# Optimization experiments

Measured on AMD Instinct MI355X. Metric: run time of the kernel, lower is better.

## Reference

```python
import jax, jax.numpy as jnp
import numpy as np

IN_DIMS = 1024
K = 8


def setup_inputs() -> dict:
    key = jax.random.key(0)
    ks = jax.random.split(key, 7)
    s = 1.0 / np.sqrt(IN_DIMS)
    x = jax.random.normal(ks[0], (8, 2048, IN_DIMS), dtype=jnp.float32)
    Wq = jax.random.uniform(ks[1], (IN_DIMS, K), jnp.float32, -s, s)
    bq = jax.random.uniform(ks[2], (K,), jnp.float32, -s, s)
    Wk = jax.random.uniform(ks[3], (IN_DIMS, K), jnp.float32, -s, s)
    bk = jax.random.uniform(ks[4], (K,), jnp.float32, -s, s)
    Wv = jax.random.uniform(ks[5], (IN_DIMS, IN_DIMS), jnp.float32, -s, s)
    bv = jax.random.uniform(ks[6], (IN_DIMS,), jnp.float32, -s, s)
    return {"x": x, "Wq": Wq, "bq": bq, "Wk": Wk, "bk": bk, "Wv": Wv, "bv": bv}


def reference(x, Wq, bq, Wk, bk, Wv, bv):
    # x: [B,S,D]; rank-k projections
    q = jnp.einsum('bsd,dk->bsk', x, Wq) + bq        # [B,S,k]
    k = jnp.einsum('bsd,dk->bsk', x, Wk) + bk        # [B,S,k]
    energy = jnp.einsum('bik,bjk->bij', q, k)        # [B,S,S] (unscaled)
    attention = jax.nn.softmax(energy, axis=-1)
    value = jnp.einsum('bsd,de->bse', x, Wv) + bv    # [B,S,D]
    out = jnp.einsum('bij,bjd->bid', attention, value)
    return (out, attention)
```

## Files before the change

### kernel.cpp

```cpp
#include <hip/hip_runtime.h>


typedef __attribute__((ext_vector_type(8))) __bf16 bf16x8;
typedef __attribute__((ext_vector_type(4))) __bf16 bf16x4;
typedef __attribute__((ext_vector_type(4))) float  f32x4;
typedef unsigned int u32;

#define GLB_CAST(p) ((const __attribute__((address_space(1))) u32*)(p))
#define LDS_CAST(p) ((__attribute__((address_space(3))) u32*)(p))

#define S_BARRIER() { __builtin_amdgcn_s_barrier(); __builtin_amdgcn_sched_barrier(0); }
#define LGKM0()     { asm volatile("s_waitcnt lgkmcnt(0)" ::: "memory"); __builtin_amdgcn_sched_barrier(0); }
#define VMCNT8()    { asm volatile("s_waitcnt vmcnt(8)" ::: "memory"); __builtin_amdgcn_sched_barrier(0); }
#define VMCNT0()    { asm volatile("s_waitcnt vmcnt(0)" ::: "memory"); __builtin_amdgcn_sched_barrier(0); }

static constexpr int    Bn   = 8;
static constexpr int    S    = 2048;
static constexpr int    Dd   = 1024;
static constexpr int    Mtot = Bn * S;
static constexpr size_t OUT0 = (size_t)Bn * S * Dd;

static constexpr size_t OFF_XBF  = 0;
static constexpr size_t OFF_WVT  = OFF_XBF + (size_t)Mtot * Dd * 2;
static constexpr size_t OFF_WQKT = OFF_WVT + (size_t)Dd * Dd * 2;
static constexpr size_t OFF_Q    = OFF_WQKT + (size_t)16 * Dd * 2;
static constexpr size_t OFF_K    = OFF_Q   + (size_t)Mtot * 8 * 4;
static constexpr size_t OFF_VT   = OFF_K   + (size_t)Mtot * 8 * 4;
static constexpr size_t OFF_ATTB = OFF_VT  + (size_t)Bn * Dd * S * 2;
static constexpr size_t WS_NEED  = OFF_ATTB + (size_t)Bn * S * S * 2;

__global__ __launch_bounds__(256) void prep_kernel(
    const float* __restrict__ x, const float* __restrict__ Wq,
    const float* __restrict__ Wk, const float* __restrict__ Wv,
    __bf16* __restrict__ xbf, __bf16* __restrict__ wvt, __bf16* __restrict__ wqkT)
{
    __shared__ float lt[64][65];
    int bid = blockIdx.x, t = threadIdx.x;
    if (bid < 4096) {
        #pragma unroll
        for (int i = 0; i < 4; ++i) {
            size_t idx4 = (size_t)i * 1048576 + (size_t)bid * 256 + t;
            f32x4 v = ((const f32x4*)x)[idx4];
            bf16x4 o;
            #pragma unroll
            for (int c = 0; c < 4; ++c) o[c] = (__bf16)v[c];
            ((bf16x4*)xbf)[idx4] = o;
        }
    } else if (bid < 4352) {
        int tile = bid - 4096;
        int tr = tile >> 4, tc = tile & 15;
        int r0 = t >> 6, c = t & 63;
        #pragma unroll
        for (int i = 0; i < 16; ++i) {
            int row = i * 4 + r0;
            lt[row][c] = Wv[(size_t)(tr * 64 + row) * 1024 + tc * 64 + c];
        }
        __syncthreads();
        #pragma unroll
        for (int i = 0; i < 16; ++i) {
            int er = i * 4 + r0;
            wvt[(size_t)(tc * 64 + er) * 1024 + tr * 64 + c] = (__bf16)lt[c][er];
        }
    } else {
        int lb = bid - 4352;
        #pragma unroll
        for (int i = 0; i < 4; ++i) {
            int idx = (lb * 4 + i) * 256 + t;
            int n = idx >> 10, d = idx & 1023;
            float v = (n < 8) ? Wq[d * 8 + n] : Wk[d * 8 + (n & 7)];
            wqkT[n * 1024 + d] = (__bf16)v;
        }
    }
}

__global__ __launch_bounds__(256) void qk_proj_kernel(
    const __bf16* __restrict__ xbf, const __bf16* __restrict__ wqkT,
    const float* __restrict__ bq, const float* __restrict__ bk,
    float* __restrict__ qb, float* __restrict__ kb)
{
    int t = threadIdx.x, l = t & 63, w = t >> 6;
    int mbase = (blockIdx.x * 4 + w) * 16;
    f32x4 acc = {0.f, 0.f, 0.f, 0.f};
    const __bf16* ar = xbf + (size_t)(mbase + (l & 15)) * 1024 + ((l >> 4) << 3);
    const __bf16* br = wqkT + (size_t)(l & 15) * 1024 + ((l >> 4) << 3);
    #pragma unroll 8
    for (int kk = 0; kk < 1024; kk += 32) {
        bf16x8 a = *(const bf16x8*)(ar + kk);
        bf16x8 b = *(const bf16x8*)(br + kk);
        acc = __builtin_amdgcn_mfma_f32_16x16x32_bf16(a, b, acc, 0, 0, 0);
    }
    int n = l & 15;
    float bias = (n < 8) ? bq[n] : bk[n & 7];
    #pragma unroll
    for (int r = 0; r < 4; ++r) {
        int m = mbase + ((l >> 4) << 2) + r;
        float v = acc[r] + bias;
        if (n < 8) qb[m * 8 + n] = v;
        else       kb[m * 8 + (n & 7)] = v;
    }
}

__global__ __launch_bounds__(256) void fused_gs_kernel(
    const __bf16* __restrict__ xbf, const __bf16* __restrict__ wvt,
    const float* __restrict__ bv,
    const float* __restrict__ qb, const float* __restrict__ kb,
    __bf16* __restrict__ vtOut, float* __restrict__ attnF,
    __bf16* __restrict__ attnB)
{
    __shared__ __align__(1024) char smem[32768];
    __shared__ float redm[4], reds[4];
    int bid = blockIdx.x, t = threadIdx.x;
    int seg = bid >> 8;
    int gid = -1, sid = -1;
    if (seg == 0) gid = bid;
    else if (seg == 1) sid = bid - 256;
    else if (seg == 2) gid = bid - 256;
    else if (seg == 3) sid = bid - 512;
    else gid = bid - 512;

    if (sid < 0) {
        int g = ((gid & 7) << 7) | (gid >> 3);
        int mblk = g >> 3, nblk = g & 7;
        int l = t & 63, wid = t >> 6;
        int wmr = wid >> 1, wnc = wid & 1;
        int lr = l & 15, lk = l >> 4;

        int srow = t >> 3;
        int ssl  = (t & 7) ^ (srow & 7);
        const __bf16* gA = xbf + (size_t)(mblk * 128 + srow) * 1024 + ssl * 8;
        const __bf16* gB = wvt + (size_t)(nblk * 128 + srow) * 1024 + ssl * 8;

        int s0 = (lk ^ (lr & 7)) << 3;
        int s1 = ((lk ^ 4) ^ (lr & 7)) << 3;
        int offA0 = (wmr * 64 + lr) * 64 + s0;
        int offA1 = (wmr * 64 + lr) * 64 + s1;
        int offB0 = (wnc * 64 + lr) * 64 + s0;
        int offB1 = (wnc * 64 + lr) * 64 + s1;

        f32x4 acc[4][4] = {};

        for (int tt = 0; tt < 16; ++tt) {
            int kk = tt * 64;
            #pragma unroll
            for (int c = 0; c < 4; ++c) {
                __builtin_amdgcn_global_load_lds(
                    GLB_CAST(gA + (size_t)c * 32 * 1024 + kk),
                    LDS_CAST(smem + c * 4096 + wid * 1024), 16, 0, 0);
                __builtin_amdgcn_global_load_lds(
                    GLB_CAST(gB + (size_t)c * 32 * 1024 + kk),
                    LDS_CAST(smem + 16384 + c * 4096 + wid * 1024), 16, 0, 0);
            }
            __syncthreads();
            const __bf16* As = (const __bf16*)smem;
            const __bf16* Bs = (const __bf16*)(smem + 16384);
            bf16x8 af[4], bfr[4];
            #pragma unroll
            for (int i = 0; i < 4; ++i) af[i]  = *(const bf16x8*)(As + offA0 + i * 1024);
            #pragma unroll
            for (int j = 0; j < 4; ++j) bfr[j] = *(const bf16x8*)(Bs + offB0 + j * 1024);
            #pragma unroll
            for (int i = 0; i < 4; ++i)
                #pragma unroll
                for (int j = 0; j < 4; ++j)
                    acc[i][j] = __builtin_amdgcn_mfma_f32_16x16x32_bf16(af[i], bfr[j], acc[i][j], 0, 0, 0);
            #pragma unroll
            for (int i = 0; i < 4; ++i) af[i]  = *(const bf16x8*)(As + offA1 + i * 1024);
            #pragma unroll
            for (int j = 0; j < 4; ++j) bfr[j] = *(const bf16x8*)(Bs + offB1 + j * 1024);
            #pragma unroll
            for (int i = 0; i < 4; ++i)
                #pragma unroll
                for (int j = 0; j < 4; ++j)
                    acc[i][j] = __builtin_amdgcn_mfma_f32_16x16x32_bf16(af[i], bfr[j], acc[i][j], 0, 0, 0);
            __syncthreads();
        }

        #pragma unroll
        for (int j = 0; j < 4; ++j) {
            int e = (nblk << 7) + wnc * 64 + j * 16 + lr;
            float bias = bv[e];
            #pragma unroll
            for (int i = 0; i < 4; ++i) {
                int m0 = (mblk << 7) + wmr * 64 + i * 16 + (lk << 2);
                int b = m0 >> 11, sA = m0 & 2047;
                bf16x4 o;
                #pragma unroll
                for (int r = 0; r < 4; ++r) o[r] = (__bf16)(acc[i][j][r] + bias);
                *(bf16x4*)&vtOut[(((size_t)(b << 10) + e) << 11) + sA] = o;
            }
        }
    } else {
        int b = sid >> 6, chunk = sid & 63;
        int l = t & 63, w = t >> 6;
        float kr[8][8];
        const float* kbb = kb + ((size_t)b << 14);
        #pragma unroll
        for (int jj = 0; jj < 8; ++jj) {
            f32x4 v0 = *(const f32x4*)(kbb + (size_t)(t * 8 + jj) * 8);
            f32x4 v1 = *(const f32x4*)(kbb + (size_t)(t * 8 + jj) * 8 + 4);
            #pragma unroll
            for (int c = 0; c < 4; ++c) { kr[jj][c] = v0[c]; kr[jj][4 + c] = v1[c]; }
        }
        const float* qrow = qb + ((size_t)b << 14);
        for (int ii = 0; ii < 32; ++ii) {
            int i = (chunk << 5) + ii;
            f32x4 q0 = *(const f32x4*)(qrow + (size_t)i * 8);
            f32x4 q1 = *(const f32x4*)(qrow + (size_t)i * 8 + 4);
            float e[8];
            #pragma unroll
            for (int jj = 0; jj < 8; ++jj) {
                float s = q0[0] * kr[jj][0];
                s = fmaf(q0[1], kr[jj][1], s);
                s = fmaf(q0[2], kr[jj][2], s);
                s = fmaf(q0[3], kr[jj][3], s);
                s = fmaf(q1[0], kr[jj][4], s);
                s = fmaf(q1[1], kr[jj][5], s);
                s = fmaf(q1[2], kr[jj][6], s);
                s = fmaf(q1[3], kr[jj][7], s);
                e[jj] = s;
            }
            float mx = e[0];
            #pragma unroll
            for (int jj = 1; jj < 8; ++jj) mx = fmaxf(mx, e[jj]);
            #pragma unroll
            for (int d = 1; d < 64; d <<= 1) mx = fmaxf(mx, __shfl_xor(mx, d));
            if (l == 0) redm[w] = mx;
            __syncthreads();
            mx = fmaxf(fmaxf(redm[0], redm[1]), fmaxf(redm[2], redm[3]));
            float p[8], sum = 0.f;
            #pragma unroll
            for (int jj = 0; jj < 8; ++jj) { p[jj] = __expf(e[jj] - mx); sum += p[jj]; }
            #pragma unroll
            for (int d = 1; d < 64; d <<= 1) sum += __shfl_xor(sum, d);
            if (l == 0) reds[w] = sum;
            __syncthreads();
            float T = (reds[0] + reds[1]) + (reds[2] + reds[3]);
            float inv = 1.0f / T;
            size_t off = (((size_t)b << 11) + i) * 2048 + (size_t)t * 8;
            f32x4 o0, o1; bf16x8 ob;
            #pragma unroll
            for (int c = 0; c < 4; ++c) {
                o0[c] = p[c] * inv; o1[c] = p[4 + c] * inv;
                ob[c] = (__bf16)o0[c]; ob[4 + c] = (__bf16)o1[c];
            }
            *(f32x4*)(attnF + off) = o0;
            *(f32x4*)(attnF + off + 4) = o1;
            *(bf16x8*)(attnB + off) = ob;
        }
    }
}

__device__ __forceinline__ void g1_stageA(const __bf16* Ab, char* smem,
    int slot, int kk, int c, int rowin, int sl8, int wid)
{
    __builtin_amdgcn_global_load_lds(
        GLB_CAST(Ab + (size_t)(c * 64 + rowin) * 2048 + kk + sl8 * 8),
        LDS_CAST(smem + slot * 65536 + c * 8192 + wid * 1024), 16, 0, 0);
}
__device__ __forceinline__ void g1_stageB(const __bf16* Bb, char* smem,
    int slot, int kk, int c, int rowin, int sl8, int wid)
{
    __builtin_amdgcn_global_load_lds(
        GLB_CAST(Bb + (size_t)(c * 64 + rowin) * 2048 + kk + sl8 * 8),
        LDS_CAST(smem + slot * 65536 + 32768 + c * 8192 + wid * 1024), 16, 0, 0);
}

__global__ __launch_bounds__(512, 2) void gemm1_kernel(
    const __bf16* __restrict__ A, const __bf16* __restrict__ Bt,
    float* __restrict__ outF)
{
    constexpr int NT = 32;
    __shared__ __align__(1024) char smem[131072];

    int bid = blockIdx.x;
    int wg = ((bid & 7) << 5) | (bid >> 3);
    int t = threadIdx.x, l = t & 63;
    int wid = t >> 6;
    int wmr = wid >> 2, wnc = wid & 3;

    int bb = wg >> 5; int r = wg & 31;
    int mblk = r >> 2, nblk = r & 3;
    const __bf16* Ab = A + (size_t)bb * S * S + (size_t)mblk * 256 * 2048;
    const __bf16* Bb = Bt + (size_t)bb * Dd * S + (size_t)nblk * 256 * 2048;

    int rowin = t >> 3;
    int sl8 = (t & 7) ^ (rowin & 7);
    int lr = l & 15, lk = l >> 4;

    f32x4 acc[8][4] = {};

    #pragma unroll
    for (int c = 0; c < 4; ++c) {
        g1_stageA(Ab, smem, 0, 0, c, rowin, sl8, wid);
        g1_stageB(Bb, smem, 0, 0, c, rowin, sl8, wid);
    }
    #pragma unroll
    for (int c = 0; c < 4; ++c) {
        g1_stageA(Ab, smem, 1, 64, c, rowin, sl8, wid);
        g1_stageB(Bb, smem, 1, 64, c, rowin, sl8, wid);
    }
    VMCNT8();
    S_BARRIER();

    for (int tt = 0; tt < NT; ++tt) {
        int s = tt & 1;
        const __bf16* Asl = (const __bf16*)(smem + s * 65536);
        const __bf16* Bsl = (const __bf16*)(smem + s * 65536 + 32768);
        bool pf = (tt + 2 < NT);
        int kk2 = (tt + 2) * 64;

        bf16x8 aLo[2][4], aHi[2][4], bLo[2][2], bHi[2][2];

        #pragma unroll
        for (int ks = 0; ks < 2; ++ks) {
            int sa = ks * 4 + lk;
            #pragma unroll
            for (int i = 0; i < 4; ++i) {
                int ra = wmr * 128 + i * 16 + lr;
                aLo[ks][i] = *(const bf16x8*)&Asl[ra * 64 + ((sa ^ (ra & 7)) << 3)];
            }
            #pragma unroll
            for (int j = 0; j < 2; ++j) {
                int rb = wnc * 64 + j * 16 + lr;
                bLo[ks][j] = *(const bf16x8*)&Bsl[rb * 64 + ((sa ^ (rb & 7)) << 3)];
            }
        }
        S_BARRIER(); LGKM0();
        __builtin_amdgcn_s_setprio(1);
        #pragma unroll
        for (int ks = 0; ks < 2; ++ks)
            #pragma unroll
            for (int i = 0; i < 4; ++i)
                #pragma unroll
                for (int j = 0; j < 2; ++j)
                    acc[i][j] = __builtin_amdgcn_mfma_f32_16x16x32_bf16(aLo[ks][i], bLo[ks][j], acc[i][j], 0, 0, 0);
        __builtin_amdgcn_s_setprio(0);
        S_BARRIER();

        #pragma unroll
        for (int ks = 0; ks < 2; ++ks) {
            int sa = ks * 4 + lk;
            #pragma unroll
            for (int j = 0; j < 2; ++j) {
                int rb = wnc * 64 + (j + 2) * 16 + lr;
                bHi[ks][j] = *(const bf16x8*)&Bsl[rb * 64 + ((sa ^ (rb & 7)) << 3)];
            }
        }
        if (pf) {
            g1_stageA(Ab, smem, s, kk2, 0, rowin, sl8, wid);
            g1_stageA(Ab, smem, s, kk2, 2, rowin, sl8, wid);
        }
        S_BARRIER(); LGKM0();
        __builtin_amdgcn_s_setprio(1);
        #pragma unroll
        for (int ks = 0; ks < 2; ++ks)
            #pragma unroll
            for (int i = 0; i < 4; ++i)
                #pragma unroll
                for (int j = 0; j < 2; ++j)
                    acc[i][2 + j] = __builtin_amdgcn_mfma_f32_16x16x32_bf16(aLo[ks][i], bHi[ks][j], acc[i][2 + j], 0, 0, 0);
        __builtin_amdgcn_s_setprio(0);
        S_BARRIER();

        #pragma unroll
        for (int ks = 0; ks < 2; ++ks) {
            int sa = ks * 4 + lk;
            #pragma unroll
            for (int i = 0; i < 4; ++i) {
                int ra = wmr * 128 + (i + 4) * 16 + lr;
                aHi[ks][i] = *(const bf16x8*)&Asl[ra * 64 + ((sa ^ (ra & 7)) << 3)];
            }
        }
        if (pf) {
            #pragma unroll
            for (int c = 0; c < 4; ++c)
                g1_stageB(Bb, smem, s, kk2, c, rowin, sl8, wid);
        }
        S_BARRIER(); LGKM0();
        __builtin_amdgcn_s_setprio(1);
        #pragma unroll
        for (int ks = 0; ks < 2; ++ks)
            #pragma unroll
            for (int i = 0; i < 4; ++i)
                #pragma unroll
                for (int j = 0; j < 2; ++j)
                    acc[4 + i][2 + j] = __builtin_amdgcn_mfma_f32_16x16x32_bf16(aHi[ks][i], bHi[ks][j], acc[4 + i][2 + j], 0, 0, 0);
        __builtin_amdgcn_s_setprio(0);
        S_BARRIER();

        if (pf) {
            g1_stageA(Ab, smem, s, kk2, 1, rowin, sl8, wid);
            g1_stageA(Ab, smem, s, kk2, 3, rowin, sl8, wid);
        }
        S_BARRIER();
        __builtin_amdgcn_s_setprio(1);
        #pragma unroll
        for (int ks = 0; ks < 2; ++ks)
            #pragma unroll
            for (int i = 0; i < 4; ++i)
                #pragma unroll
                for (int j = 0; j < 2; ++j)
                    acc[4 + i][j] = __builtin_amdgcn_mfma_f32_16x16x32_bf16(aHi[ks][i], bLo[ks][j], acc[4 + i][j], 0, 0, 0);
        __builtin_amdgcn_s_setprio(0);

        if (tt == NT - 1) break;
        S_BARRIER();
        if (pf) { VMCNT8(); } else { VMCNT0(); }
        S_BARRIER();
    }

    float* ob = outF + (size_t)bb * S * Dd;
    #pragma unroll
    for (int i = 0; i < 8; ++i) {
        int m0 = (mblk << 8) + wmr * 128 + i * 16 + (lk << 2);
        #pragma unroll
        for (int j = 0; j < 4; ++j) {
            int e = (nblk << 8) + wnc * 64 + j * 16 + lr;
            #pragma unroll
            for (int r = 0; r < 4; ++r)
                ob[(size_t)(m0 + r) * 1024 + e] = acc[i][j][r];
        }
    }
}

extern "C" void kernel_launch(void* const* d_in, const int* in_sizes, int n_in,
                              void* d_out, int out_size, void* d_ws, size_t ws_size,
                              hipStream_t stream)
{
    const float* x  = (const float*)d_in[0];
    const float* Wq = (const float*)d_in[1];
    const float* bq = (const float*)d_in[2];
    const float* Wk = (const float*)d_in[3];
    const float* bk = (const float*)d_in[4];
    const float* Wv = (const float*)d_in[5];
    const float* bv = (const float*)d_in[6];

    float* outp  = (float*)d_out;
    float* attnF = outp + OUT0;

    if (ws_size < WS_NEED) return;
    char* ws = (char*)d_ws;
    __bf16* xbf   = (__bf16*)(ws + OFF_XBF);
    __bf16* wvt   = (__bf16*)(ws + OFF_WVT);
    __bf16* wqkT  = (__bf16*)(ws + OFF_WQKT);
    float*  qbuf  = (float*)(ws + OFF_Q);
    float*  kbuf  = (float*)(ws + OFF_K);
    __bf16* vt    = (__bf16*)(ws + OFF_VT);
    __bf16* attnB = (__bf16*)(ws + OFF_ATTB);

    prep_kernel<<<4368, 256, 0, stream>>>(x, Wq, Wk, Wv, xbf, wvt, wqkT);
    qk_proj_kernel<<<256, 256, 0, stream>>>(xbf, wqkT, bq, bk, qbuf, kbuf);
    fused_gs_kernel<<<1536, 256, 0, stream>>>(xbf, wvt, bv, qbuf, kbuf, vt, attnF, attnB);
    gemm1_kernel<<<256, 512, 0, stream>>>(attnB, vt, outp);
}
```

Before: 187.1 us.

## Fuse QK projection into prep and overlap fp32 attention writes with gemm

Removes the separate QK projection kernel by computing the rank-16 projection directly from fp32 x inside prep_kernel. The fp32 attention output store is moved out of the softmax kernel into gemm1, which reloads bf16 attention rows and writes them as fp32 while its MFMA loop runs. This aims to hide the large fp32 attention write behind compute and cut a launch, but makes the fp32 attention output carry bf16 rounding and complicates the vmcnt accounting.

```diff
diff --git a/kernel.cpp b/kernel.cpp
--- a/kernel.cpp
+++ b/kernel.cpp
@@ -11,6 +11,7 @@
 
 #define S_BARRIER() { __builtin_amdgcn_s_barrier(); __builtin_amdgcn_sched_barrier(0); }
 #define LGKM0()     { asm volatile("s_waitcnt lgkmcnt(0)" ::: "memory"); __builtin_amdgcn_sched_barrier(0); }
+#define VMCNT9()    { asm volatile("s_waitcnt vmcnt(9)" ::: "memory"); __builtin_amdgcn_sched_barrier(0); }
 #define VMCNT8()    { asm volatile("s_waitcnt vmcnt(8)" ::: "memory"); __builtin_amdgcn_sched_barrier(0); }
 #define VMCNT0()    { asm volatile("s_waitcnt vmcnt(0)" ::: "memory"); __builtin_amdgcn_sched_barrier(0); }
 
@@ -22,8 +23,7 @@
 
 static constexpr size_t OFF_XBF  = 0;
 static constexpr size_t OFF_WVT  = OFF_XBF + (size_t)Mtot * Dd * 2;
-static constexpr size_t OFF_WQKT = OFF_WVT + (size_t)Dd * Dd * 2;
-static constexpr size_t OFF_Q    = OFF_WQKT + (size_t)16 * Dd * 2;
+static constexpr size_t OFF_Q    = OFF_WVT + (size_t)Dd * Dd * 2;
 static constexpr size_t OFF_K    = OFF_Q   + (size_t)Mtot * 8 * 4;
 static constexpr size_t OFF_VT   = OFF_K   + (size_t)Mtot * 8 * 4;
 static constexpr size_t OFF_ATTB = OFF_VT  + (size_t)Bn * Dd * S * 2;
@@ -32,22 +32,41 @@
 __global__ __launch_bounds__(256) void prep_kernel(
     const float* __restrict__ x, const float* __restrict__ Wq,
     const float* __restrict__ Wk, const float* __restrict__ Wv,
-    __bf16* __restrict__ xbf, __bf16* __restrict__ wvt, __bf16* __restrict__ wqkT)
+    const float* __restrict__ bq, const float* __restrict__ bk,
+    __bf16* __restrict__ xbf, __bf16* __restrict__ wvt,
+    float* __restrict__ qb, float* __restrict__ kb)
 {
     __shared__ float lt[64][65];
     int bid = blockIdx.x, t = threadIdx.x;
-    if (bid < 4096) {
-        #pragma unroll
-        for (int i = 0; i < 4; ++i) {
-            size_t idx4 = (size_t)i * 1048576 + (size_t)bid * 256 + t;
-            f32x4 v = ((const f32x4*)x)[idx4];
-            bf16x4 o;
-            #pragma unroll
-            for (int c = 0; c < 4; ++c) o[c] = (__bf16)v[c];
-            ((bf16x4*)xbf)[idx4] = o;
-        }
-    } else if (bid < 4352) {
-        int tile = bid - 4096;
+    if (bid < 256) {
+        int l = t & 63, w = t >> 6;
+        int mbase = (bid * 4 + w) * 16;
+        int n = l & 15;
+        int dbase = (l >> 4) << 3;
+        const float* xr = x + (size_t)(mbase + n) * 1024 + dbase;
+        const float* wcol = (n < 8) ? (Wq + n) : (Wk + (n & 7));
+        f32x4 acc = {0.f, 0.f, 0.f, 0.f};
+        #pragma unroll 4
+        for (int kk = 0; kk < 1024; kk += 32) {
+            f32x4 a0 = *(const f32x4*)(xr + kk);
+            f32x4 a1 = *(const f32x4*)(xr + kk + 4);
+            bf16x8 a, b;
+            #pragma unroll
+            for (int c = 0; c < 4; ++c) { a[c] = (__bf16)a0[c]; a[4 + c] = (__bf16)a1[c]; }
+            #pragma unroll
+            for (int u = 0; u < 8; ++u) b[u] = (__bf16)wcol[(size_t)(dbase + kk + u) * 8];
+            acc = __builtin_amdgcn_mfma_f32_16x16x32_bf16(a, b, acc, 0, 0, 0);
+        }
+        float bias = (n < 8) ? bq[n] : bk[n & 7];
+        #pragma unroll
+        for (int r = 0; r < 4; ++r) {
+            int m = mbase + ((l >> 4) << 2) + r;
+            float v = acc[r] + bias;
+            if (n < 8) qb[m * 8 + n] = v;
+            else       kb[m * 8 + (n & 7)] = v;
+        }
+    } else if (bid < 512) {
+        int tile = bid - 256;
         int tr = tile >> 4, tc = tile & 15;
         int r0 = t >> 6, c = t & 63;
         #pragma unroll
@@ -62,41 +81,16 @@
             wvt[(size_t)(tc * 64 + er) * 1024 + tr * 64 + c] = (__bf16)lt[c][er];
         }
     } else {
-        int lb = bid - 4352;
+        int bid2 = bid - 512;
         #pragma unroll
         for (int i = 0; i < 4; ++i) {
-            int idx = (lb * 4 + i) * 256 + t;
-            int n = idx >> 10, d = idx & 1023;
-            float v = (n < 8) ? Wq[d * 8 + n] : Wk[d * 8 + (n & 7)];
-            wqkT[n * 1024 + d] = (__bf16)v;
-        }
-    }
-}
-
-__global__ __launch_bounds__(256) void qk_proj_kernel(
-    const __bf16* __restrict__ xbf, const __bf16* __restrict__ wqkT,
-    const float* __restrict__ bq, const float* __restrict__ bk,
-    float* __restrict__ qb, float* __restrict__ kb)
-{
-    int t = threadIdx.x, l = t & 63, w = t >> 6;
-    int mbase = (blockIdx.x * 4 + w) * 16;
-    f32x4 acc = {0.f, 0.f, 0.f, 0.f};
-    const __bf16* ar = xbf + (size_t)(mbase + (l & 15)) * 1024 + ((l >> 4) << 3);
-    const __bf16* br = wqkT + (size_t)(l & 15) * 1024 + ((l >> 4) << 3);
-    #pragma unroll 8
-    for (int kk = 0; kk < 1024; kk += 32) {
-        bf16x8 a = *(const bf16x8*)(ar + kk);
-        bf16x8 b = *(const bf16x8*)(br + kk);
-        acc = __builtin_amdgcn_mfma_f32_16x16x32_bf16(a, b, acc, 0, 0, 0);
-    }
-    int n = l & 15;
-    float bias = (n < 8) ? bq[n] : bk[n & 7];
-    #pragma unroll
-    for (int r = 0; r < 4; ++r) {
-        int m = mbase + ((l >> 4) << 2) + r;
-        float v = acc[r] + bias;
-        if (n < 8) qb[m * 8 + n] = v;
-        else       kb[m * 8 + (n & 7)] = v;
+            size_t idx4 = (size_t)i * 1048576 + (size_t)bid2 * 256 + t;
+            f32x4 v = ((const f32x4*)x)[idx4];
+            bf16x4 o;
+            #pragma unroll
+            for (int c = 0; c < 4; ++c) o[c] = (__bf16)v[c];
+            ((bf16x4*)xbf)[idx4] = o;
+        }
     }
 }
 
@@ -104,8 +98,7 @@
     const __bf16* __restrict__ xbf, const __bf16* __restrict__ wvt,
     const float* __restrict__ bv,
     const float* __restrict__ qb, const float* __restrict__ kb,
-    __bf16* __restrict__ vtOut, float* __restrict__ attnF,
-    __bf16* __restrict__ attnB)
+    __bf16* __restrict__ vtOut, __bf16* __restrict__ attnB)
 {
     __shared__ __align__(1024) char smem[32768];
     __shared__ float redm[4], reds[4];
@@ -237,14 +230,11 @@
             float T = (reds[0] + reds[1]) + (reds[2] + reds[3]);
             float inv = 1.0f / T;
             size_t off = (((size_t)b << 11) + i) * 2048 + (size_t)t * 8;
-            f32x4 o0, o1; bf16x8 ob;
+            bf16x8 ob;
             #pragma unroll
             for (int c = 0; c < 4; ++c) {
-                o0[c] = p[c] * inv; o1[c] = p[4 + c] * inv;
-                ob[c] = (__bf16)o0[c]; ob[4 + c] = (__bf16)o1[c];
-            }
-            *(f32x4*)(attnF + off) = o0;
-            *(f32x4*)(attnF + off + 4) = o1;
+                ob[c] = (__bf16)(p[c] * inv); ob[4 + c] = (__bf16)(p[4 + c] * inv);
+            }
             *(bf16x8*)(attnB + off) = ob;
         }
     }
@@ -267,7 +257,7 @@
 
 __global__ __launch_bounds__(512, 2) void gemm1_kernel(
     const __bf16* __restrict__ A, const __bf16* __restrict__ Bt,
-    float* __restrict__ outF)
+    float* __restrict__ outF, float* __restrict__ attnF)
 {
     constexpr int NT = 32;
     __shared__ __align__(1024) char smem[131072];
@@ -286,6 +276,12 @@
     int rowin = t >> 3;
     int sl8 = (t & 7) ^ (rowin & 7);
     int lr = l & 15, lk = l >> 4;
+
+    int crow = nblk * 64 + (t >> 3);
+    int ccol = (t & 7) * 8;
+    const __bf16* cpSrc = Ab + (size_t)crow * 2048 + ccol;
+    float* cpDst = attnF + ((size_t)bb << 22) + ((size_t)(mblk * 256 + crow) << 11) + ccol;
+    bf16x8 pv;
 
     f32x4 acc[8][4] = {};
 
@@ -309,6 +305,17 @@
         bool pf = (tt + 2 < NT);
         int kk2 = (tt + 2) * 64;
 
+        if (tt >= 2) {
+            f32x4 c0, c1;
+            #pragma unroll
+            for (int c = 0; c < 4; ++c) { c0[c] = (float)pv[c]; c1[c] = (float)pv[4 + c]; }
+            *(f32x4*)(cpDst + (tt - 2) * 64) = c0;
+            *(f32x4*)(cpDst + (tt - 2) * 64 + 4) = c1;
+        }
+        if (tt >= 1) {
+            pv = *(const bf16x8*)(cpSrc + (tt - 1) * 64);
+        }
+
         bf16x8 aLo[2][4], aHi[2][4], bLo[2][2], bHi[2][2];
 
         #pragma unroll
@@ -405,8 +412,25 @@
 
         if (tt == NT - 1) break;
         S_BARRIER();
-        if (pf) { VMCNT8(); } else { VMCNT0(); }
-        S_BARRIER();
+        if (pf) {
+            if (tt == 0) { VMCNT8(); } else { VMCNT9(); }
+        } else {
+            VMCNT0();
+        }
+        S_BARRIER();
+    }
+
+    {
+        f32x4 c0, c1;
+        #pragma unroll
+        for (int c = 0; c < 4; ++c) { c0[c] = (float)pv[c]; c1[c] = (float)pv[4 + c]; }
+        *(f32x4*)(cpDst + (NT - 2) * 64) = c0;
+        *(f32x4*)(cpDst + (NT - 2) * 64 + 4) = c1;
+        bf16x8 lastv = *(const bf16x8*)(cpSrc + (NT - 1) * 64);
+        #pragma unroll
+        for (int c = 0; c < 4; ++c) { c0[c] = (float)lastv[c]; c1[c] = (float)lastv[4 + c]; }
+        *(f32x4*)(cpDst + (NT - 1) * 64) = c0;
+        *(f32x4*)(cpDst + (NT - 1) * 64 + 4) = c1;
     }
 
     float* ob = outF + (size_t)bb * S * Dd;
@@ -442,14 +466,12 @@
     char* ws = (char*)d_ws;
     __bf16* xbf   = (__bf16*)(ws + OFF_XBF);
     __bf16* wvt   = (__bf16*)(ws + OFF_WVT);
-    __bf16* wqkT  = (__bf16*)(ws + OFF_WQKT);
     float*  qbuf  = (float*)(ws + OFF_Q);
     float*  kbuf  = (float*)(ws + OFF_K);
     __bf16* vt    = (__bf16*)(ws + OFF_VT);
     __bf16* attnB = (__bf16*)(ws + OFF_ATTB);
 
-    prep_kernel<<<4368, 256, 0, stream>>>(x, Wq, Wk, Wv, xbf, wvt, wqkT);
-    qk_proj_kernel<<<256, 256, 0, stream>>>(xbf, wqkT, bq, bk, qbuf, kbuf);
-    fused_gs_kernel<<<1536, 256, 0, stream>>>(xbf, wvt, bv, qbuf, kbuf, vt, attnF, attnB);
-    gemm1_kernel<<<256, 512, 0, stream>>>(attnB, vt, outp);
-}
+    prep_kernel<<<4608, 256, 0, stream>>>(x, Wq, Wk, Wv, bq, bk, xbf, wvt, qbuf, kbuf);
+    fused_gs_kernel<<<1536, 256, 0, stream>>>(xbf, wvt, bv, qbuf, kbuf, vt, attnB);
+    gemm1_kernel<<<256, 512, 0, stream>>>(attnB, vt, outp, attnF);
+}
```

Result: no change. 189.6 us (median of 2 runs) (+1.4%).
